# Kernel optimization log

Measured on AMD Instinct MI355X. Metric: run time of the kernel, lower is better.

## Reference

```python
import jax, jax.numpy as jnp
import numpy as np

N = 400000
D = 512
NS = 50000


def setup_inputs() -> dict:
    key = jax.random.key(0)
    k1, k2, k3, k4 = jax.random.split(key, 4)
    x = jax.random.normal(k1, (N, D), dtype=jnp.float32)
    index = jax.random.randint(k2, (N,), 0, NS, dtype=jnp.int64)
    Wg = jax.random.normal(k3, (D, 1), dtype=jnp.float32) / np.sqrt(D)
    bg = jnp.zeros((1,), dtype=jnp.float32)
    Wm = jax.random.normal(k4, (D, D), dtype=jnp.float32) / np.sqrt(D)
    bm = jnp.zeros((D,), dtype=jnp.float32)
    return {"x": x, "index": index, "Wg": Wg, "bg": bg, "Wm": Wm, "bm": bm,
            "num_segments": NS}


def reference(x, index, Wg, bg, Wm, bm, num_segments):
    # gate_nn: Linear(D, 1)
    gate = x @ Wg + bg                                   # [N, 1]
    # segment softmax over nodes sharing an index (stable via segment max)
    gmax = jax.ops.segment_max(gate, index, num_segments=num_segments)  # [NS, 1]
    gate = jnp.exp(gate - gmax[index])                   # [N, 1]
    gsum = jax.ops.segment_sum(gate, index, num_segments=num_segments)  # [NS, 1]
    gate = gate / (gsum[index] + 1e-10)                  # [N, 1]
    # message_nn: Linear(D, D)
    m = x @ Wm + bm                                      # [N, D]
    out = jax.ops.segment_sum(gate * m, index, num_segments=num_segments)  # [NS, D]
    return out
```

## Files before the change

### kernel.cpp

```cpp
#include <hip/hip_runtime.h>
#include <hip/hip_bf16.h>

#define NROWS 400000
#define DDIM  512
#define NSEG  50000
#define CAP   64

typedef __bf16 bf16x8 __attribute__((ext_vector_type(8)));
typedef float  f32x4_t __attribute__((ext_vector_type(4)));

#define GLOAD_LDS16(gsrc, ldst)                                                  \
    __builtin_amdgcn_global_load_lds(                                            \
        (const __attribute__((address_space(1))) void*)(gsrc),                   \
        (__attribute__((address_space(3))) void*)(ldst), 16, 0, 0)


__global__ __launch_bounds__(256)
void scatter_prep(const int* __restrict__ idx, int* __restrict__ counts,
                  int* __restrict__ slots,
                  const float* __restrict__ Wm, __bf16* __restrict__ WmT) {
    __shared__ float tile[64 * 65];
    int b = blockIdx.x;
    int t = threadIdx.x;
    if (b < 1563) {
        int r = b * 256 + t;
        if (r < NROWS) {
            int s = idx[r];
            int p = atomicAdd(&counts[s], 1);
            slots[s * CAP + p] = r;
        }
    } else {
        int tb = b - 1563;
        int kt = tb >> 3, nt = tb & 7;
        int cc = t & 63, rg = t >> 6;
#pragma unroll
        for (int it = 0; it < 16; ++it) {
            int rr = it * 4 + rg;
            tile[rr * 65 + cc] = Wm[(size_t)(kt * 64 + rr) * 512 + nt * 64 + cc];
        }
        __syncthreads();
#pragma unroll
        for (int it = 0; it < 16; ++it) {
            int nn = it * 4 + rg;
            WmT[(size_t)(nt * 64 + nn) * 512 + kt * 64 + cc] =
                (__bf16)tile[cc * 65 + nn];
        }
    }
}


__global__ __launch_bounds__(256)
void pool_kernel(const float* __restrict__ x,
                 const int* __restrict__ counts,
                 const int* __restrict__ slots,
                 const float* __restrict__ Wg,
                 const float* __restrict__ bgp,
                 __bf16* __restrict__ px,
                 float* __restrict__ scaleB) {
    const int lane = threadIdx.x & 63;
    const int s = blockIdx.x * 4 + (threadIdx.x >> 6);
    const f32x4_t wg0 = *(const f32x4_t*)(Wg + lane * 8);
    const f32x4_t wg1 = *(const f32x4_t*)(Wg + lane * 8 + 4);
    const float bg = bgp[0];
    const int n   = counts[s];
    const int* sid = slots + s * CAP;

    f32x4_t acc0 = {0.f, 0.f, 0.f, 0.f}, acc1 = acc0;
    float gs = 0.f;

    f32x4_t r0a = acc0, r0b = acc0, r1a = acc0, r1b = acc0;
    f32x4_t r2a = acc0, r2b = acc0, r3a = acc0, r3b = acc0;

#define LOADR(k, u0, u1)                                                        \
    {   const float* xr = x + (size_t)sid[k] * DDIM + lane * 8;                 \
        u0 = __builtin_nontemporal_load((const f32x4_t*)xr);                    \
        u1 = __builtin_nontemporal_load((const f32x4_t*)(xr + 4)); }
#define COMPR(u0, u1)                                                           \
    {   float p = u0.x * wg0.x + u0.y * wg0.y + u0.z * wg0.z + u0.w * wg0.w     \
                + u1.x * wg1.x + u1.y * wg1.y + u1.z * wg1.z + u1.w * wg1.w;    \
        p += __shfl_xor(p, 1);  p += __shfl_xor(p, 2);  p += __shfl_xor(p, 4);  \
        p += __shfl_xor(p, 8);  p += __shfl_xor(p, 16); p += __shfl_xor(p, 32); \
        float e = __expf(p + bg);                                               \
        gs += e; acc0 += e * u0; acc1 += e * u1; }

    if (n > 0) LOADR(0, r0a, r0b);
    if (n > 1) LOADR(1, r1a, r1b);
    if (n > 2) LOADR(2, r2a, r2b);
    if (n > 3) LOADR(3, r3a, r3b);

    int k = 0;
    for (; k + 8 <= n; k += 4) {
        COMPR(r0a, r0b); LOADR(k + 4, r0a, r0b);
        COMPR(r1a, r1b); LOADR(k + 5, r1a, r1b);
        COMPR(r2a, r2b); LOADR(k + 6, r2a, r2b);
        COMPR(r3a, r3b); LOADR(k + 7, r3a, r3b);
    }
    {
        int rem = n - k;
        if (rem > 0) COMPR(r0a, r0b);
        if (rem > 4) LOADR(k + 4, r0a, r0b);
        if (rem > 1) COMPR(r1a, r1b);
        if (rem > 5) LOADR(k + 5, r1a, r1b);
        if (rem > 2) COMPR(r2a, r2b);
        if (rem > 6) LOADR(k + 6, r2a, r2b);
        if (rem > 3) COMPR(r3a, r3b);
        if (rem > 4) COMPR(r0a, r0b);
        if (rem > 5) COMPR(r1a, r1b);
        if (rem > 6) COMPR(r2a, r2b);
    }
#undef LOADR
#undef COMPR

    float inv = 1.f / (gs + 1e-10f);
    bf16x8 o;
    o[0] = (__bf16)(acc0.x * inv); o[1] = (__bf16)(acc0.y * inv);
    o[2] = (__bf16)(acc0.z * inv); o[3] = (__bf16)(acc0.w * inv);
    o[4] = (__bf16)(acc1.x * inv); o[5] = (__bf16)(acc1.y * inv);
    o[6] = (__bf16)(acc1.z * inv); o[7] = (__bf16)(acc1.w * inv);
    *(bf16x8*)(px + (size_t)s * DDIM + lane * 8) = o;
    if (lane == 0) scaleB[s] = gs * inv;
}


__global__ __launch_bounds__(256)
void gemm_out(const __bf16* __restrict__ px,
              const __bf16* __restrict__ WmT,
              const float* __restrict__ bm,
              const float* __restrict__ scaleB,
              float* __restrict__ out) {
    __shared__ __align__(16) __bf16 As[128 * 64];
    __shared__ __align__(16) __bf16 Bs[128 * 64];

    const int t     = threadIdx.x;
    const int lane  = t & 63;
    const int w     = t >> 6;
    const int ntile = blockIdx.x & 3;
    const int mtile = blockIdx.x >> 2;

    const int kq = lane & 15;
    const int rq = lane >> 4;
    const int wr = w >> 1;
    const int wc = w & 1;

    const char* srcA[4];
    const char* srcB[4];
    int ldsOff[4];
#pragma unroll
    for (int q = 0; q < 4; ++q) {
        int base = w * 4096 + q * 1024;
        int L = base + lane * 16;
        int r = L >> 7;
        int c = (L & 127) ^ ((r & 7) << 4);
        ldsOff[q] = base;
        int growA = mtile * 128 + r; if (growA >= NSEG) growA = NSEG - 1;
        srcA[q] = (const char*)px + (size_t)growA * 1024 + c;
        srcB[q] = (const char*)WmT + (size_t)(ntile * 128 + r) * 1024 + c;
    }

    f32x4_t acc[4][4];
#pragma unroll
    for (int i = 0; i < 4; ++i)
#pragma unroll
        for (int j = 0; j < 4; ++j)
            acc[i][j] = f32x4_t{0.f, 0.f, 0.f, 0.f};

    for (int ks = 0; ks < 8; ++ks) {
#pragma unroll
        for (int q = 0; q < 4; ++q) {
            GLOAD_LDS16(srcA[q] + ks * 128, (char*)As + ldsOff[q]);
            GLOAD_LDS16(srcB[q] + ks * 128, (char*)Bs + ldsOff[q]);
        }
        asm volatile("s_waitcnt vmcnt(0)" ::: "memory");
        __builtin_amdgcn_s_barrier();
#pragma unroll
        for (int kk = 0; kk < 2; ++kk) {
            int kbyte = rq * 16 + kk * 64;
            bf16x8 a[4], b[4];
#pragma unroll
            for (int mi = 0; mi < 4; ++mi) {
                int r = wr * 64 + mi * 16 + kq;
                a[mi] = *(const bf16x8*)((char*)As + ((r * 128 + kbyte) ^ ((r & 7) << 4)));
            }
#pragma unroll
            for (int ni = 0; ni < 4; ++ni) {
                int c = wc * 64 + ni * 16 + kq;
                b[ni] = *(const bf16x8*)((char*)Bs + ((c * 128 + kbyte) ^ ((c & 7) << 4)));
            }
#pragma unroll
            for (int mi = 0; mi < 4; ++mi)
#pragma unroll
                for (int ni = 0; ni < 4; ++ni)
                    acc[mi][ni] = __builtin_amdgcn_mfma_f32_16x16x32_bf16(
                        a[mi], b[ni], acc[mi][ni], 0, 0, 0);
        }
        __builtin_amdgcn_s_barrier();
    }

#pragma unroll
    for (int mi = 0; mi < 4; ++mi) {
#pragma unroll
        for (int j = 0; j < 4; ++j) {
            int rrow = wr * 64 + mi * 16 + rq * 4 + j;
            int grow = mtile * 128 + rrow;
            if (grow < NSEG) {
                float sb = scaleB[grow];
                float* op = out + (size_t)grow * DDIM + ntile * 128 + wc * 64 + kq;
                const float* bp = bm + ntile * 128 + wc * 64 + kq;
#pragma unroll
                for (int ni = 0; ni < 4; ++ni)
                    __builtin_nontemporal_store(acc[mi][ni][j] + bp[ni * 16] * sb,
                                                op + ni * 16);
            }
        }
    }
}

extern "C" void kernel_launch(void* const* d_in, const int* in_sizes, int n_in,
                              void* d_out, int out_size, void* d_ws, size_t ws_size,
                              hipStream_t stream) {
    const float* x   = (const float*)d_in[0];
    const int*   idx = (const int*)d_in[1];
    const float* Wg  = (const float*)d_in[2];
    const float* bg  = (const float*)d_in[3];
    const float* Wm  = (const float*)d_in[4];
    const float* bm  = (const float*)d_in[5];
    float* out = (float*)d_out;

    char* W = (char*)d_ws;
    int*    counts = (int*)   (W + 0);
    float*  scaleB = (float*) (W + 200704);
    __bf16* WmT    = (__bf16*)(W + 401408);
    int*    slots  = (int*)   (W + 925696);
    __bf16* px     = (__bf16*)(W + 13725696);

    hipMemsetAsync(counts, 0, NSEG * sizeof(int), stream);

    scatter_prep<<<1563 + 64, 256, 0, stream>>>(idx, counts, slots, Wm, WmT);
    pool_kernel<<<NSEG / 4, 256, 0, stream>>>(x, counts, slots, Wg, bg, px, scaleB);

    int mtiles = (NSEG + 127) / 128;
    gemm_out<<<mtiles * 4, 256, 0, stream>>>(px, WmT, bm, scaleB, out);
}
```

Baseline: 277.4 us.

## Fuse all stages into one persistent cooperative kernel with grid syncs

```diff
diff --git a/kernel.cpp b/kernel.cpp
--- a/kernel.cpp
+++ b/kernel.cpp
@@ -1,5 +1,8 @@
 #include <hip/hip_runtime.h>
 #include <hip/hip_bf16.h>
+#include <hip/hip_cooperative_groups.h>
+
+namespace cg = cooperative_groups;
 
 #define NROWS 400000
 #define DDIM  512
@@ -13,6 +16,239 @@
     __builtin_amdgcn_global_load_lds(                                            \
         (const __attribute__((address_space(1))) void*)(gsrc),                   \
         (__attribute__((address_space(3))) void*)(ldst), 16, 0, 0)
+
+
+__device__ __forceinline__ void transpose_tile_body(int tb, float* tile, int t,
+                                                    const float* __restrict__ Wm,
+                                                    __bf16* __restrict__ WmT) {
+    int kt = tb >> 3, nt = tb & 7;
+    int cc = t & 63, rg = t >> 6;
+#pragma unroll
+    for (int it = 0; it < 16; ++it) {
+        int rr = it * 4 + rg;
+        tile[rr * 65 + cc] = Wm[(size_t)(kt * 64 + rr) * 512 + nt * 64 + cc];
+    }
+    __syncthreads();
+#pragma unroll
+    for (int it = 0; it < 16; ++it) {
+        int nn = it * 4 + rg;
+        WmT[(size_t)(nt * 64 + nn) * 512 + kt * 64 + cc] = (__bf16)tile[cc * 65 + nn];
+    }
+    __syncthreads();
+}
+
+__device__ __forceinline__ void pool_seg_body(int s, int lane,
+                                              const float* __restrict__ x,
+                                              const int* __restrict__ counts,
+                                              const int* __restrict__ slots,
+                                              const f32x4_t wg0, const f32x4_t wg1,
+                                              float bg,
+                                              __bf16* __restrict__ px,
+                                              float* __restrict__ scaleB) {
+    const int n = counts[s];
+    const int* sid = slots + s * CAP;
+    f32x4_t acc0 = {0.f, 0.f, 0.f, 0.f}, acc1 = acc0;
+    float gs = 0.f;
+    f32x4_t r0a = acc0, r0b = acc0, r1a = acc0, r1b = acc0;
+    f32x4_t r2a = acc0, r2b = acc0, r3a = acc0, r3b = acc0;
+
+#define LOADR(k, u0, u1)                                                        \
+    {   const float* xr = x + (size_t)sid[k] * DDIM + lane * 8;                 \
+        u0 = __builtin_nontemporal_load((const f32x4_t*)xr);                    \
+        u1 = __builtin_nontemporal_load((const f32x4_t*)(xr + 4)); }
+#define COMPR(u0, u1)                                                           \
+    {   float p = u0.x * wg0.x + u0.y * wg0.y + u0.z * wg0.z + u0.w * wg0.w     \
+                + u1.x * wg1.x + u1.y * wg1.y + u1.z * wg1.z + u1.w * wg1.w;    \
+        p += __shfl_xor(p, 1);  p += __shfl_xor(p, 2);  p += __shfl_xor(p, 4);  \
+        p += __shfl_xor(p, 8);  p += __shfl_xor(p, 16); p += __shfl_xor(p, 32); \
+        float e = __expf(p + bg);                                               \
+        gs += e; acc0 += e * u0; acc1 += e * u1; }
+
+    if (n > 0) LOADR(0, r0a, r0b);
+    if (n > 1) LOADR(1, r1a, r1b);
+    if (n > 2) LOADR(2, r2a, r2b);
+    if (n > 3) LOADR(3, r3a, r3b);
+    int k = 0;
+    for (; k + 8 <= n; k += 4) {
+        COMPR(r0a, r0b); LOADR(k + 4, r0a, r0b);
+        COMPR(r1a, r1b); LOADR(k + 5, r1a, r1b);
+        COMPR(r2a, r2b); LOADR(k + 6, r2a, r2b);
+        COMPR(r3a, r3b); LOADR(k + 7, r3a, r3b);
+    }
+    {
+        int rem = n - k;
+        if (rem > 0) COMPR(r0a, r0b);
+        if (rem > 4) LOADR(k + 4, r0a, r0b);
+        if (rem > 1) COMPR(r1a, r1b);
+        if (rem > 5) LOADR(k + 5, r1a, r1b);
+        if (rem > 2) COMPR(r2a, r2b);
+        if (rem > 6) LOADR(k + 6, r2a, r2b);
+        if (rem > 3) COMPR(r3a, r3b);
+        if (rem > 4) COMPR(r0a, r0b);
+        if (rem > 5) COMPR(r1a, r1b);
+        if (rem > 6) COMPR(r2a, r2b);
+    }
+#undef LOADR
+#undef COMPR
+    float inv = 1.f / (gs + 1e-10f);
+    bf16x8 o;
+    o[0] = (__bf16)(acc0.x * inv); o[1] = (__bf16)(acc0.y * inv);
+    o[2] = (__bf16)(acc0.z * inv); o[3] = (__bf16)(acc0.w * inv);
+    o[4] = (__bf16)(acc1.x * inv); o[5] = (__bf16)(acc1.y * inv);
+    o[6] = (__bf16)(acc1.z * inv); o[7] = (__bf16)(acc1.w * inv);
+    *(bf16x8*)(px + (size_t)s * DDIM + lane * 8) = o;
+    if (lane == 0) scaleB[s] = gs * inv;
+}
+
+__device__ __forceinline__ void gemm_tile_body(int mtile, int ntile, int lane, int w,
+                                               __bf16* As, __bf16* Bs,
+                                               const __bf16* __restrict__ px,
+                                               const __bf16* __restrict__ WmT,
+                                               const float* __restrict__ bm,
+                                               const float* __restrict__ scaleB,
+                                               float* __restrict__ out) {
+    const int kq = lane & 15;
+    const int rq = lane >> 4;
+    const int wr = w >> 1;
+    const int wc = w & 1;
+
+    const char* srcA[4];
+    const char* srcB[4];
+    int ldsOff[4];
+#pragma unroll
+    for (int q = 0; q < 4; ++q) {
+        int base = w * 4096 + q * 1024;
+        int L = base + lane * 16;
+        int r = L >> 7;
+        int c = (L & 127) ^ ((r & 7) << 4);
+        ldsOff[q] = base;
+        int growA = mtile * 128 + r; if (growA >= NSEG) growA = NSEG - 1;
+        srcA[q] = (const char*)px + (size_t)growA * 1024 + c;
+        srcB[q] = (const char*)WmT + (size_t)(ntile * 128 + r) * 1024 + c;
+    }
+
+    f32x4_t acc[4][4];
+#pragma unroll
+    for (int i = 0; i < 4; ++i)
+#pragma unroll
+        for (int j = 0; j < 4; ++j)
+            acc[i][j] = f32x4_t{0.f, 0.f, 0.f, 0.f};
+
+    for (int ks = 0; ks < 8; ++ks) {
+#pragma unroll
+        for (int q = 0; q < 4; ++q) {
+            GLOAD_LDS16(srcA[q] + ks * 128, (char*)As + ldsOff[q]);
+            GLOAD_LDS16(srcB[q] + ks * 128, (char*)Bs + ldsOff[q]);
+        }
+        asm volatile("s_waitcnt vmcnt(0)" ::: "memory");
+        __builtin_amdgcn_s_barrier();
+#pragma unroll
+        for (int kk = 0; kk < 2; ++kk) {
+            int kbyte = rq * 16 + kk * 64;
+            bf16x8 a[4], bfr[4];
+#pragma unroll
+            for (int mi = 0; mi < 4; ++mi) {
+                int r = wr * 64 + mi * 16 + kq;
+                a[mi] = *(const bf16x8*)((char*)As + ((r * 128 + kbyte) ^ ((r & 7) << 4)));
+            }
+#pragma unroll
+            for (int ni = 0; ni < 4; ++ni) {
+                int c = wc * 64 + ni * 16 + kq;
+                bfr[ni] = *(const bf16x8*)((char*)Bs + ((c * 128 + kbyte) ^ ((c & 7) << 4)));
+            }
+#pragma unroll
+            for (int mi = 0; mi < 4; ++mi)
+#pragma unroll
+                for (int ni = 0; ni < 4; ++ni)
+                    acc[mi][ni] = __builtin_amdgcn_mfma_f32_16x16x32_bf16(
+                        a[mi], bfr[ni], acc[mi][ni], 0, 0, 0);
+        }
+        __builtin_amdgcn_s_barrier();
+    }
+
+#pragma unroll
+    for (int mi = 0; mi < 4; ++mi) {
+#pragma unroll
+        for (int jj = 0; jj < 4; ++jj) {
+            int rrow = wr * 64 + mi * 16 + rq * 4 + jj;
+            int grow = mtile * 128 + rrow;
+            if (grow < NSEG) {
+                float sb = scaleB[grow];
+                float* op = out + (size_t)grow * DDIM + ntile * 128 + wc * 64 + kq;
+                const float* bp = bm + ntile * 128 + wc * 64 + kq;
+#pragma unroll
+                for (int ni = 0; ni < 4; ++ni)
+                    __builtin_nontemporal_store(acc[mi][ni][jj] + bp[ni * 16] * sb,
+                                                op + ni * 16);
+            }
+        }
+    }
+}
+
+
+__global__ __launch_bounds__(256, 2)
+void fused_all(const float* __restrict__ x,
+               const int* __restrict__ idx,
+               const float* __restrict__ Wg,
+               const float* __restrict__ bgp,
+               const float* __restrict__ Wm,
+               const float* __restrict__ bm,
+               int* __restrict__ counts,
+               int* __restrict__ slots,
+               __bf16* __restrict__ WmT,
+               __bf16* __restrict__ px,
+               float* __restrict__ scaleB,
+               float* __restrict__ out) {
+    __shared__ __align__(16) char smem[32768];
+    float* tile = (float*)smem;
+    __bf16* As  = (__bf16*)smem;
+    __bf16* Bs  = (__bf16*)(smem + 16384);
+
+    cg::grid_group grid = cg::this_grid();
+    const int nb   = gridDim.x;
+    const int b    = blockIdx.x;
+    const int t    = threadIdx.x;
+    const int lane = t & 63;
+    const int w    = t >> 6;
+
+    for (int i = b * 256 + t; i < NSEG; i += nb * 256) counts[i] = 0;
+    grid.sync();
+
+    for (int wi = b; wi < 1563 + 64; wi += nb) {
+        if (wi < 1563) {
+            int r = wi * 256 + t;
+            if (r < NROWS) {
+                int s = idx[r];
+                int p = atomicAdd(&counts[s], 1);
+                slots[s * CAP + p] = r;
+            }
+        } else {
+            transpose_tile_body(wi - 1563, tile, t, Wm, WmT);
+        }
+    }
+    grid.sync();
+
+    {
+        const f32x4_t wg0 = *(const f32x4_t*)(Wg + lane * 8);
+        const f32x4_t wg1 = *(const f32x4_t*)(Wg + lane * 8 + 4);
+        const float bg = bgp[0];
+        for (int g = b; g < NSEG / 4; g += nb)
+            pool_seg_body(g * 4 + w, lane, x, counts, slots, wg0, wg1, bg, px, scaleB);
+    }
+    grid.sync();
+
+    {
+        const int xk = b & 7;
+        const int j  = b >> 3;
+        const int nM = (xk < 7) ? 49 : 48;
+        const int nT = nM * 4;
+        for (int e = j; e < nT; e += (nb >> 3)) {
+            gemm_tile_body(xk + 8 * (e >> 2), e & 3, lane, w, As, Bs,
+                           px, WmT, bm, scaleB, out);
+            __syncthreads();
+        }
+    }
+}
 
 
 __global__ __launch_bounds__(256)
@@ -30,24 +266,9 @@
             slots[s * CAP + p] = r;
         }
     } else {
-        int tb = b - 1563;
-        int kt = tb >> 3, nt = tb & 7;
-        int cc = t & 63, rg = t >> 6;
-#pragma unroll
-        for (int it = 0; it < 16; ++it) {
-            int rr = it * 4 + rg;
-            tile[rr * 65 + cc] = Wm[(size_t)(kt * 64 + rr) * 512 + nt * 64 + cc];
-        }
-        __syncthreads();
-#pragma unroll
-        for (int it = 0; it < 16; ++it) {
-            int nn = it * 4 + rg;
-            WmT[(size_t)(nt * 64 + nn) * 512 + kt * 64 + cc] =
-                (__bf16)tile[cc * 65 + nn];
-        }
-    }
-}
-
+        transpose_tile_body(b - 1563, tile, t, Wm, WmT);
+    }
+}
 
 __global__ __launch_bounds__(256)
 void pool_kernel(const float* __restrict__ x,
@@ -58,69 +279,11 @@
                  __bf16* __restrict__ px,
                  float* __restrict__ scaleB) {
     const int lane = threadIdx.x & 63;
-    const int s = blockIdx.x * 4 + (threadIdx.x >> 6);
     const f32x4_t wg0 = *(const f32x4_t*)(Wg + lane * 8);
     const f32x4_t wg1 = *(const f32x4_t*)(Wg + lane * 8 + 4);
-    const float bg = bgp[0];
-    const int n   = counts[s];
-    const int* sid = slots + s * CAP;
-
-    f32x4_t acc0 = {0.f, 0.f, 0.f, 0.f}, acc1 = acc0;
-    float gs = 0.f;
-
-    f32x4_t r0a = acc0, r0b = acc0, r1a = acc0, r1b = acc0;
-    f32x4_t r2a = acc0, r2b = acc0, r3a = acc0, r3b = acc0;
-
-#define LOADR(k, u0, u1)                                                        \
-    {   const float* xr = x + (size_t)sid[k] * DDIM + lane * 8;                 \
-        u0 = __builtin_nontemporal_load((const f32x4_t*)xr);                    \
-        u1 = __builtin_nontemporal_load((const f32x4_t*)(xr + 4)); }
-#define COMPR(u0, u1)                                                           \
-    {   float p = u0.x * wg0.x + u0.y * wg0.y + u0.z * wg0.z + u0.w * wg0.w     \
-                + u1.x * wg1.x + u1.y * wg1.y + u1.z * wg1.z + u1.w * wg1.w;    \
-        p += __shfl_xor(p, 1);  p += __shfl_xor(p, 2);  p += __shfl_xor(p, 4);  \
-        p += __shfl_xor(p, 8);  p += __shfl_xor(p, 16); p += __shfl_xor(p, 32); \
-        float e = __expf(p + bg);                                               \
-        gs += e; acc0 += e * u0; acc1 += e * u1; }
-
-    if (n > 0) LOADR(0, r0a, r0b);
-    if (n > 1) LOADR(1, r1a, r1b);
-    if (n > 2) LOADR(2, r2a, r2b);
-    if (n > 3) LOADR(3, r3a, r3b);
-
-    int k = 0;
-    for (; k + 8 <= n; k += 4) {
-        COMPR(r0a, r0b); LOADR(k + 4, r0a, r0b);
-        COMPR(r1a, r1b); LOADR(k + 5, r1a, r1b);
-        COMPR(r2a, r2b); LOADR(k + 6, r2a, r2b);
-        COMPR(r3a, r3b); LOADR(k + 7, r3a, r3b);
-    }
-    {
-        int rem = n - k;
-        if (rem > 0) COMPR(r0a, r0b);
-        if (rem > 4) LOADR(k + 4, r0a, r0b);
-        if (rem > 1) COMPR(r1a, r1b);
-        if (rem > 5) LOADR(k + 5, r1a, r1b);
-        if (rem > 2) COMPR(r2a, r2b);
-        if (rem > 6) LOADR(k + 6, r2a, r2b);
-        if (rem > 3) COMPR(r3a, r3b);
-        if (rem > 4) COMPR(r0a, r0b);
-        if (rem > 5) COMPR(r1a, r1b);
-        if (rem > 6) COMPR(r2a, r2b);
-    }
-#undef LOADR
-#undef COMPR
-
-    float inv = 1.f / (gs + 1e-10f);
-    bf16x8 o;
-    o[0] = (__bf16)(acc0.x * inv); o[1] = (__bf16)(acc0.y * inv);
-    o[2] = (__bf16)(acc0.z * inv); o[3] = (__bf16)(acc0.w * inv);
-    o[4] = (__bf16)(acc1.x * inv); o[5] = (__bf16)(acc1.y * inv);
-    o[6] = (__bf16)(acc1.z * inv); o[7] = (__bf16)(acc1.w * inv);
-    *(bf16x8*)(px + (size_t)s * DDIM + lane * 8) = o;
-    if (lane == 0) scaleB[s] = gs * inv;
-}
-
+    pool_seg_body(blockIdx.x * 4 + (threadIdx.x >> 6), lane, x, counts, slots,
+                  wg0, wg1, bgp[0], px, scaleB);
+}
 
 __global__ __launch_bounds__(256)
 void gemm_out(const __bf16* __restrict__ px,
@@ -130,89 +293,12 @@
               float* __restrict__ out) {
     __shared__ __align__(16) __bf16 As[128 * 64];
     __shared__ __align__(16) __bf16 Bs[128 * 64];
-
-    const int t     = threadIdx.x;
-    const int lane  = t & 63;
-    const int w     = t >> 6;
-    const int ntile = blockIdx.x & 3;
-    const int mtile = blockIdx.x >> 2;
-
-    const int kq = lane & 15;
-    const int rq = lane >> 4;
-    const int wr = w >> 1;
-    const int wc = w & 1;
-
-    const char* srcA[4];
-    const char* srcB[4];
-    int ldsOff[4];
-#pragma unroll
-    for (int q = 0; q < 4; ++q) {
-        int base = w * 4096 + q * 1024;
-        int L = base + lane * 16;
-        int r = L >> 7;
-        int c = (L & 127) ^ ((r & 7) << 4);
-        ldsOff[q] = base;
-        int growA = mtile * 128 + r; if (growA >= NSEG) growA = NSEG - 1;
-        srcA[q] = (const char*)px + (size_t)growA * 1024 + c;
-        srcB[q] = (const char*)WmT + (size_t)(ntile * 128 + r) * 1024 + c;
-    }
-
-    f32x4_t acc[4][4];
-#pragma unroll
-    for (int i = 0; i < 4; ++i)
-#pragma unroll
-        for (int j = 0; j < 4; ++j)
-            acc[i][j] = f32x4_t{0.f, 0.f, 0.f, 0.f};
-
-    for (int ks = 0; ks < 8; ++ks) {
-#pragma unroll
-        for (int q = 0; q < 4; ++q) {
-            GLOAD_LDS16(srcA[q] + ks * 128, (char*)As + ldsOff[q]);
-            GLOAD_LDS16(srcB[q] + ks * 128, (char*)Bs + ldsOff[q]);
-        }
-        asm volatile("s_waitcnt vmcnt(0)" ::: "memory");
-        __builtin_amdgcn_s_barrier();
-#pragma unroll
-        for (int kk = 0; kk < 2; ++kk) {
-            int kbyte = rq * 16 + kk * 64;
-            bf16x8 a[4], b[4];
-#pragma unroll
-            for (int mi = 0; mi < 4; ++mi) {
-                int r = wr * 64 + mi * 16 + kq;
-                a[mi] = *(const bf16x8*)((char*)As + ((r * 128 + kbyte) ^ ((r & 7) << 4)));
-            }
-#pragma unroll
-            for (int ni = 0; ni < 4; ++ni) {
-                int c = wc * 64 + ni * 16 + kq;
-                b[ni] = *(const bf16x8*)((char*)Bs + ((c * 128 + kbyte) ^ ((c & 7) << 4)));
-            }
-#pragma unroll
-            for (int mi = 0; mi < 4; ++mi)
-#pragma unroll
-                for (int ni = 0; ni < 4; ++ni)
-                    acc[mi][ni] = __builtin_amdgcn_mfma_f32_16x16x32_bf16(
-                        a[mi], b[ni], acc[mi][ni], 0, 0, 0);
-        }
-        __builtin_amdgcn_s_barrier();
-    }
-
-#pragma unroll
-    for (int mi = 0; mi < 4; ++mi) {
-#pragma unroll
-        for (int j = 0; j < 4; ++j) {
-            int rrow = wr * 64 + mi * 16 + rq * 4 + j;
-            int grow = mtile * 128 + rrow;
-            if (grow < NSEG) {
-                float sb = scaleB[grow];
-                float* op = out + (size_t)grow * DDIM + ntile * 128 + wc * 64 + kq;
-                const float* bp = bm + ntile * 128 + wc * 64 + kq;
-#pragma unroll
-                for (int ni = 0; ni < 4; ++ni)
-                    __builtin_nontemporal_store(acc[mi][ni][j] + bp[ni * 16] * sb,
-                                                op + ni * 16);
-            }
-        }
-    }
+    const int xk = blockIdx.x & 7;
+    const int j  = blockIdx.x >> 3;
+    const int mtile = xk + 8 * (j >> 2);
+    if (mtile >= 391) return;
+    gemm_tile_body(mtile, j & 3, threadIdx.x & 63, threadIdx.x >> 6, As, Bs,
+                   px, WmT, bm, scaleB, out);
 }
 
 extern "C" void kernel_launch(void* const* d_in, const int* in_sizes, int n_in,
@@ -233,11 +319,30 @@
     int*    slots  = (int*)   (W + 925696);
     __bf16* px     = (__bf16*)(W + 13725696);
 
-    hipMemsetAsync(counts, 0, NSEG * sizeof(int), stream);
-
-    scatter_prep<<<1563 + 64, 256, 0, stream>>>(idx, counts, slots, Wm, WmT);
-    pool_kernel<<<NSEG / 4, 256, 0, stream>>>(x, counts, slots, Wg, bg, px, scaleB);
-
-    int mtiles = (NSEG + 127) / 128;
-    gemm_out<<<mtiles * 4, 256, 0, stream>>>(px, WmT, bm, scaleB, out);
-}
+    int blocksPerCU = 0;
+    hipError_t qerr = hipOccupancyMaxActiveBlocksPerMultiprocessor(
+        &blocksPerCU, fused_all, 256, 0);
+    int nb = 0;
+    if (qerr == hipSuccess && blocksPerCU > 0) {
+        long cand = (long)blocksPerCU * 256;
+        if (cand > 1024) cand = 1024;
+        nb = (int)(cand & ~7L);
+    }
+
+    bool ok = false;
+    if (nb >= 8) {
+        void* args[] = {(void*)&x, (void*)&idx, (void*)&Wg, (void*)&bg, (void*)&Wm,
+                        (void*)&bm, (void*)&counts, (void*)&slots, (void*)&WmT,
+                        (void*)&px, (void*)&scaleB, (void*)&out};
+        hipError_t lerr = hipLaunchCooperativeKernel((void*)fused_all, dim3(nb),
+                                                     dim3(256), args, 0, stream);
+        ok = (lerr == hipSuccess);
+    }
+
+    if (!ok) {
+        hipMemsetAsync(counts, 0, NSEG * sizeof(int), stream);
+        scatter_prep<<<1563 + 64, 256, 0, stream>>>(idx, counts, slots, Wm, WmT);
+        pool_kernel<<<NSEG / 4, 256, 0, stream>>>(x, counts, slots, Wg, bg, px, scaleB);
+        gemm_out<<<8 * 49 * 4, 256, 0, stream>>>(px, WmT, bm, scaleB, out);
+    }
+}
```

Result: slower. 513.6 us (+85.2%).
